# Optimization experiments

Measured on AMD Instinct MI355X. Metric: run time of the kernel, lower is better.

## Reference

```python
import jax, jax.numpy as jnp
import numpy as np

HEADS = 8
DIM_HEAD = 64
DIM = 512
NUM_BANDS = 32
MAX_FREQ = 32.0
NORM_SCALE = 10.0
RPE_DIM = (NUM_BANDS * 2 + 1) * 2  # 130


def setup_inputs() -> dict:
    key = jax.random.key(0)
    ks = jax.random.split(key, 9)
    B, N = 2, 512
    inner = HEADS * DIM_HEAD
    h2 = HEADS * 2
    inp = {
        "x": jax.random.normal(ks[0], (B, N, DIM), dtype=jnp.float32),
        "positions": jax.random.uniform(ks[1], (B, N, 2), dtype=jnp.float32),
        "W_qkv": jax.random.normal(ks[2], (DIM, 3 * inner), dtype=jnp.float32) / np.sqrt(DIM),
        "W_out": jax.random.normal(ks[3], (inner, DIM), dtype=jnp.float32) / np.sqrt(inner),
        "b_out": jnp.zeros((DIM,), dtype=jnp.float32),
        "rpe_W1": jax.random.normal(ks[4], (RPE_DIM, h2), dtype=jnp.float32) / np.sqrt(RPE_DIM),
        "rpe_b1": jnp.zeros((h2,), dtype=jnp.float32),
        "rpe_W2": jax.random.normal(ks[5], (h2, HEADS), dtype=jnp.float32) / np.sqrt(h2),
        "rpe_b2": jnp.zeros((HEADS,), dtype=jnp.float32),
    }
    return inp


def _fourier_encode(x):
    # x: [...], returns [..., 2*NUM_BANDS+1]
    freqs = jnp.linspace(1.0, MAX_FREQ, NUM_BANDS, dtype=x.dtype)
    angles = x[..., None] * freqs * jnp.pi
    return jnp.concatenate([x[..., None], jnp.sin(angles), jnp.cos(angles)], axis=-1)


def _rpe_bias(positions, W1, b1, W2, b2):
    # positions: [B, N, 2] -> bias [B, H, N, N]
    delta = positions[:, None, :, :] - positions[:, :, None, :]  # key_pos_j - query_pos_i
    dx = delta[..., 0] / NORM_SCALE
    dy = delta[..., 1] / NORM_SCALE
    dx = dx / (1.0 + jnp.abs(dx))
    dy = dy / (1.0 + jnp.abs(dy))
    feats = jnp.concatenate([_fourier_encode(dx), _fourier_encode(dy)], axis=-1)  # [B,N,N,130]
    h = jax.nn.gelu(feats @ W1 + b1, approximate=False)
    bias = h @ W2 + b2  # [B, N, N, H]
    return jnp.transpose(bias, (0, 3, 1, 2))  # [B, H, N, N]


def reference(x, positions, W_qkv, W_out, b_out, rpe_W1, rpe_b1, rpe_W2, rpe_b2):
    B, N, _ = x.shape
    H, d = HEADS, DIM_HEAD
    scale = d ** (-0.5)
    qkv = x @ W_qkv  # [B, N, 3*H*d]
    q, k, v = jnp.split(qkv, 3, axis=-1)
    q = q.reshape(B, N, H, d)
    k = k.reshape(B, N, H, d)
    v = v.reshape(B, N, H, d)
    scores = jnp.einsum('bihd,bjhd->bhij', q, k) * scale
    scores = scores + _rpe_bias(positions, rpe_W1, rpe_b1, rpe_W2, rpe_b2)
    attn = jax.nn.softmax(scores, axis=-1)
    out = jnp.einsum('bhij,bjhd->bihd', attn, v).reshape(B, N, H * d)
    return out @ W_out + b_out
```

## Files before the change

### kernel.cpp

```cpp
#include <hip/hip_runtime.h>
#include <hip/hip_fp16.h>
#include <math.h>

typedef __attribute__((ext_vector_type(8))) _Float16 f16x8;
typedef __attribute__((ext_vector_type(4))) float f32x4;

#define TBL 512
#define UMAXV (1.0f/11.0f)

__device__ __forceinline__ int swq(int row, int q) {
  return row * 64 + ((q ^ (row & 7)) << 3);
}
__device__ __forceinline__ f16x8 cvt8(float4 a, float4 b) {
  f16x8 r;
  r[0] = (_Float16)a.x; r[1] = (_Float16)a.y;
  r[2] = (_Float16)a.z; r[3] = (_Float16)a.w;
  r[4] = (_Float16)b.x; r[5] = (_Float16)b.y;
  r[6] = (_Float16)b.z; r[7] = (_Float16)b.w;
  return r;
}

__global__ __launch_bounds__(256) void k_prep(
    const float* __restrict__ Wqkv, const float* __restrict__ Wout,
    const float* __restrict__ W1, const float* __restrict__ b1,
    _Float16* __restrict__ Wt, _Float16* __restrict__ Wot,
    __half* __restrict__ Tx, __half* __restrict__ Ty) {
  __shared__ float Tt[32 * 33];
  const int t = threadIdx.x;
  const int bid = blockIdx.x;
  if (bid >= 1024) {
    int gid = (bid - 1024) * 256 + t;
    int e = gid >> 5, c = gid & 31;
    float u = -UMAXV + (2.0f * UMAXV) * (float)e / (float)(TBL - 1);
    const int xpart = (c < 16);
    const int col = c & 15;
    const int base = xpart ? 0 : 65;
    float sum = u * W1[base * 16 + col] + (xpart ? b1[col] : 0.0f);
    float s1, c1;
    sincosf(u * 3.14159265358979323846f, &s1, &c1);
    float sk = s1, ck = c1;
    for (int k = 1; k <= 32; ++k) {
      sum += sk * W1[(base + k) * 16 + col] + ck * W1[(base + 32 + k) * 16 + col];
      float ns = sk * c1 + ck * s1;
      ck = ck * c1 - sk * s1;
      sk = ns;
    }
    (xpart ? Tx : Ty)[e * 16 + col] = __float2half(sum);
    return;
  }
  int k0, n0, ncols;
  const float* W;
  _Float16* O;
  if (bid < 768) {
    k0 = (bid / 48) * 32; n0 = (bid % 48) * 32; ncols = 1536;
    W = Wqkv; O = Wt;
  } else {
    int tile = bid - 768;
    k0 = (tile / 16) * 32; n0 = (tile % 16) * 32; ncols = 512;
    W = Wout; O = Wot;
  }
  {
    int kl = t >> 3, nl = (t & 7) * 4;
    float4 v = *(const float4*)&W[(k0 + kl) * ncols + n0 + nl];
    Tt[kl * 33 + nl + 0] = v.x;
    Tt[kl * 33 + nl + 1] = v.y;
    Tt[kl * 33 + nl + 2] = v.z;
    Tt[kl * 33 + nl + 3] = v.w;
  }
  __syncthreads();
  {
    int nl = t >> 3, kq = (t & 7) * 4;
    ushort4 h;
    h.x = __builtin_bit_cast(unsigned short, (_Float16)Tt[(kq + 0) * 33 + nl]);
    h.y = __builtin_bit_cast(unsigned short, (_Float16)Tt[(kq + 1) * 33 + nl]);
    h.z = __builtin_bit_cast(unsigned short, (_Float16)Tt[(kq + 2) * 33 + nl]);
    h.w = __builtin_bit_cast(unsigned short, (_Float16)Tt[(kq + 3) * 33 + nl]);
    *(ushort4*)&O[(n0 + nl) * 512 + k0 + kq] = h;
  }
}

__global__ __launch_bounds__(512) void k_fused(
    const float* __restrict__ x, const _Float16* __restrict__ Wt,
    _Float16* __restrict__ q16, _Float16* __restrict__ k16,
    _Float16* __restrict__ vt16,
    const float* __restrict__ pos,
    const __half* __restrict__ Tx, const __half* __restrict__ Ty,
    const float* __restrict__ W2, const float* __restrict__ b2,
    _Float16* __restrict__ bias) {
  __shared__ __align__(16) unsigned short SM[16384];
  const int bid = blockIdx.x;
  const int t = threadIdx.x;

  if (bid < 192) {
    const int gb = (bid & 7) * 24 + (bid >> 3);
    _Float16* Ah = (_Float16*)SM;
    _Float16* Bh = (_Float16*)SM + 8192;
    const int mt = gb / 24, nt = gb % 24;
    const int m0 = mt * 128, n0 = nt * 64;
    const int w = t >> 6, lane = t & 63, blk = lane >> 4, jc = lane & 15;
    const int mw = (w & 3) * 32, nw = (w >> 2) * 32;
    const int sa = t >> 3, sq = t & 7;

    f32x4 acc[2][2];
    #pragma unroll
    for (int i = 0; i < 2; ++i)
      #pragma unroll
      for (int j = 0; j < 2; ++j) acc[i][j] = f32x4{0.f, 0.f, 0.f, 0.f};

    float4 pax[2][2][2];
    f16x8 pbv[2];
    #pragma unroll
    for (int s = 0; s < 2; ++s) {
      #pragma unroll
      for (int c = 0; c < 2; ++c) {
        const float* xp = &x[(m0 + sa + c * 64) * 512 + s * 64 + sq * 8];
        pax[s][c][0] = *(const float4*)xp;
        pax[s][c][1] = *(const float4*)(xp + 4);
      }
      pbv[s] = *(const f16x8*)&Wt[(n0 + sa) * 512 + s * 64 + sq * 8];
    }

    for (int it = 0; it < 8; ++it) {
      const int slot = it & 1;
      #pragma unroll
      for (int c = 0; c < 2; ++c)
        *(f16x8*)&Ah[swq(sa + c * 64, sq)] = cvt8(pax[slot][c][0], pax[slot][c][1]);
      *(f16x8*)&Bh[swq(sa, sq)] = pbv[slot];
      __syncthreads();
      if (it < 6) {
        int k0 = (it + 2) * 64;
        #pragma unroll
        for (int c = 0; c < 2; ++c) {
          const float* xp = &x[(m0 + sa + c * 64) * 512 + k0 + sq * 8];
          pax[slot][c][0] = *(const float4*)xp;
          pax[slot][c][1] = *(const float4*)(xp + 4);
        }
        pbv[slot] = *(const f16x8*)&Wt[(n0 + sa) * 512 + k0 + sq * 8];
      }
      #pragma unroll
      for (int h = 0; h < 2; ++h) {
        int q = h * 4 + blk;
        f16x8 a0 = *(const f16x8*)&Ah[swq(mw + jc, q)];
        f16x8 a1 = *(const f16x8*)&Ah[swq(mw + 16 + jc, q)];
        f16x8 b0 = *(const f16x8*)&Bh[swq(nw + jc, q)];
        f16x8 b1 = *(const f16x8*)&Bh[swq(nw + 16 + jc, q)];
        acc[0][0] = __builtin_amdgcn_mfma_f32_16x16x32_f16(a0, b0, acc[0][0], 0, 0, 0);
        acc[0][1] = __builtin_amdgcn_mfma_f32_16x16x32_f16(a0, b1, acc[0][1], 0, 0, 0);
        acc[1][0] = __builtin_amdgcn_mfma_f32_16x16x32_f16(a1, b0, acc[1][0], 0, 0, 0);
        acc[1][1] = __builtin_amdgcn_mfma_f32_16x16x32_f16(a1, b1, acc[1][1], 0, 0, 0);
      }
      __syncthreads();
    }
    const int sec = n0 >> 9;
    const int hh_ = (n0 >> 6) & 7;
    if (sec < 2) {
      _Float16* dst = (sec == 0) ? q16 : k16;
      const float scl = (sec == 0) ? 0.125f : 1.0f;
      #pragma unroll
      for (int i = 0; i < 2; ++i)
        #pragma unroll
        for (int j = 0; j < 2; ++j)
          #pragma unroll
          for (int r = 0; r < 4; ++r) {
            int tok = m0 + mw + i * 16 + blk * 4 + r;
            int b = tok >> 9, nn = tok & 511;
            int d = nw + j * 16 + jc;
            dst[((b * 8 + hh_) * 512 + nn) * 64 + d] = (_Float16)(acc[i][j][r] * scl);
          }
    } else {
      _Float16* T = (_Float16*)SM;
      #pragma unroll
      for (int i = 0; i < 2; ++i)
        #pragma unroll
        for (int j = 0; j < 2; ++j)
          #pragma unroll
          for (int r = 0; r < 4; ++r)
            T[(nw + j * 16 + jc) * 136 + mw + i * 16 + blk * 4 + r] =
                (_Float16)acc[i][j][r];
      __syncthreads();
      const int d = t >> 3, tq = t & 7;
      const int b = m0 >> 9, nb = m0 & 511;
      #pragma unroll
      for (int c = 0; c < 2; ++c) {
        int qd = tq + c * 8;
        f16x8 vv = *(const f16x8*)&T[d * 136 + qd * 8];
        *(f16x8*)&vt16[((b * 8 + hh_) * 64 + d) * 512 + nb + qd * 8] = vv;
      }
    }
    return;
  }

  const int gid = (bid - 192) * 512 + t;
  const int b = gid >> 18;
  const int i = (gid >> 9) & 511;
  const int j = gid & 511;
  const float pix = pos[(b * 512 + i) * 2 + 0];
  const float piy = pos[(b * 512 + i) * 2 + 1];
  const float pjx = pos[(b * 512 + j) * 2 + 0];
  const float pjy = pos[(b * 512 + j) * 2 + 1];
  float txv = (pjx - pix) * 0.1f; float ux = txv / (1.0f + fabsf(txv));
  float tyv = (pjy - piy) * 0.1f; float uy = tyv / (1.0f + fabsf(tyv));
  const float invstep = (float)(TBL - 1) / (2.0f * UMAXV);
  float fx = (ux + UMAXV) * invstep;
  int ix = (int)fx; ix = min(max(ix, 0), TBL - 2);
  float wx = fx - (float)ix;
  float fy = (uy + UMAXV) * invstep;
  int iy = (int)fy; iy = min(max(iy, 0), TBL - 2);
  float wy = fy - (float)iy;

  __half hx0[16], hx1[16], hy0[16], hy1[16];
  *(uint4*)&hx0[0] = *(const uint4*)&Tx[ix * 16];
  *(uint4*)&hx0[8] = *(const uint4*)&Tx[ix * 16 + 8];
  *(uint4*)&hx1[0] = *(const uint4*)&Tx[(ix + 1) * 16];
  *(uint4*)&hx1[8] = *(const uint4*)&Tx[(ix + 1) * 16 + 8];
  *(uint4*)&hy0[0] = *(const uint4*)&Ty[iy * 16];
  *(uint4*)&hy0[8] = *(const uint4*)&Ty[iy * 16 + 8];
  *(uint4*)&hy1[0] = *(const uint4*)&Ty[(iy + 1) * 16];
  *(uint4*)&hy1[8] = *(const uint4*)&Ty[(iy + 1) * 16 + 8];

  float o[8];
  #pragma unroll
  for (int c = 0; c < 8; ++c) o[c] = b2[c];
  #pragma unroll
  for (int r = 0; r < 16; ++r) {
    float ax = __half2float(hx0[r]);
    float bx = __half2float(hx1[r]);
    float ay = __half2float(hy0[r]);
    float by = __half2float(hy1[r]);
    float hv = fmaf(wx, bx - ax, ax) + fmaf(wy, by - ay, ay);
    float z = hv * 0.70710678118654752f;
    float az = fabsf(z);
    float tt = __builtin_amdgcn_rcpf(fmaf(0.3275911f, az, 1.0f));
    float poly = ((((1.061405429f * tt - 1.453152027f) * tt + 1.421413741f) * tt
                   - 0.284496736f) * tt + 0.254829592f) * tt;
    float ex = __expf(-z * z);
    float erfv = copysignf(fmaf(-poly, ex, 1.0f), z);
    float g = 0.5f * hv * (1.0f + erfv);
    #pragma unroll
    for (int c = 0; c < 8; ++c)
      o[c] = fmaf(g, W2[r * 8 + c], o[c]);
  }
  #pragma unroll
  for (int c = 0; c < 8; ++c)
    bias[((size_t)(b * 8 + c) * 512 + i) * 512 + j] = (_Float16)o[c];
}

__global__ __launch_bounds__(512) void k_attn(
    const _Float16* __restrict__ q16, const _Float16* __restrict__ k16,
    const _Float16* __restrict__ vt16, const _Float16* __restrict__ bias,
    _Float16* __restrict__ ao16) {
  __shared__ __align__(16) _Float16 psu[8 * 512];
  __shared__ __align__(16) float olds[8 * 16 * 65];
  __shared__ float mls[8 * 16 * 2];
  _Float16* bst = (_Float16*)olds;

  const int lb = (blockIdx.x & 7) * 64 + (blockIdx.x >> 3);
  const int it = lb & 31, h = (lb >> 5) & 7, b = lb >> 8;
  const int i0 = it * 16;
  const int bh = b * 8 + h;
  const int tid = threadIdx.x;
  const int w = tid >> 6, lane = tid & 63;
  const int blk = lane >> 4, jc = lane & 15;

  {
    const _Float16* bgp = bias + ((size_t)(bh * 512 + i0)) * 512;
    int brow = tid >> 5, bc = (tid & 31) * 16;
    *(f16x8*)&bst[brow * 520 + bc]     = *(const f16x8*)&bgp[brow * 512 + bc];
    *(f16x8*)&bst[brow * 520 + bc + 8] = *(const f16x8*)&bgp[brow * 512 + bc + 8];
  }

  const int qoff = (bh * 512 + i0 + jc) * 64 + blk * 8;
  const f16x8 qa0 = *(const f16x8*)&q16[qoff];
  const f16x8 qa1 = *(const f16x8*)&q16[qoff + 32];

  const int j00 = w * 64;
  f16x8 k0A0, k0A1, k0B0, k0B1, v0[4];
  {
    const int rA = (bh * 512 + j00 + jc) * 64 + blk * 8;
    const int rB = rA + 16 * 64;
    k0A0 = *(const f16x8*)&k16[rA];
    k0A1 = *(const f16x8*)&k16[rA + 32];
    k0B0 = *(const f16x8*)&k16[rB];
    k0B1 = *(const f16x8*)&k16[rB + 32];
    #pragma unroll
    for (int dt = 0; dt < 4; ++dt)
      v0[dt] = *(const f16x8*)&vt16[(bh * 64 + dt * 16 + jc) * 512 + j00 + blk * 8];
  }

  float m[4] = {-1e30f, -1e30f, -1e30f, -1e30f};
  float l[4] = {0.f, 0.f, 0.f, 0.f};
  f32x4 o[4];
  #pragma unroll
  for (int dt = 0; dt < 4; ++dt) o[dt] = f32x4{0.f, 0.f, 0.f, 0.f};

  _Float16* pw = &psu[w * 512];
  __syncthreads();

  f32x4 aA = {0.f, 0.f, 0.f, 0.f};
  aA = __builtin_amdgcn_mfma_f32_16x16x32_f16(qa0, k0A0, aA, 0, 0, 0);
  aA = __builtin_amdgcn_mfma_f32_16x16x32_f16(qa1, k0A1, aA, 0, 0, 0);
  f32x4 aB = {0.f, 0.f, 0.f, 0.f};
  aB = __builtin_amdgcn_mfma_f32_16x16x32_f16(qa0, k0B0, aB, 0, 0, 0);
  aB = __builtin_amdgcn_mfma_f32_16x16x32_f16(qa1, k0B1, aB, 0, 0, 0);

  const int j01 = w * 64 + 32;
  f16x8 k1A0, k1A1, k1B0, k1B1, v1[4];
  {
    const int rA = (bh * 512 + j01 + jc) * 64 + blk * 8;
    const int rB = rA + 16 * 64;
    k1A0 = *(const f16x8*)&k16[rA];
    k1A1 = *(const f16x8*)&k16[rA + 32];
    k1B0 = *(const f16x8*)&k16[rB];
    k1B1 = *(const f16x8*)&k16[rB + 32];
    #pragma unroll
    for (int dt = 0; dt < 4; ++dt)
      v1[dt] = *(const f16x8*)&vt16[(bh * 64 + dt * 16 + jc) * 512 + j01 + blk * 8];
  }

  {
    float sA[4], sB[4], sc[4];
    #pragma unroll
    for (int r = 0; r < 4; ++r) {
      const int br = (blk * 4 + r) * 520;
      sA[r] = aA[r] + (float)bst[br + j00 + jc];
      sB[r] = aB[r] + (float)bst[br + j00 + 16 + jc];
    }
    #pragma unroll
    for (int r = 0; r < 4; ++r) {
      float mx = fmaxf(sA[r], sB[r]);
      mx = fmaxf(mx, __shfl_xor(mx, 1, 64));
      mx = fmaxf(mx, __shfl_xor(mx, 2, 64));
      mx = fmaxf(mx, __shfl_xor(mx, 4, 64));
      mx = fmaxf(mx, __shfl_xor(mx, 8, 64));
      float mn = fmaxf(m[r], mx);
      sc[r] = __expf(m[r] - mn);
      m[r] = mn;
      float pA = __expf(sA[r] - mn);
      float pB = __expf(sB[r] - mn);
      float ps = pA + pB;
      ps += __shfl_xor(ps, 1, 64);
      ps += __shfl_xor(ps, 2, 64);
      ps += __shfl_xor(ps, 4, 64);
      ps += __shfl_xor(ps, 8, 64);
      l[r] = l[r] * sc[r] + ps;
      pw[(blk * 4 + r) * 32 + jc] = (_Float16)pA;
      pw[(blk * 4 + r) * 32 + 16 + jc] = (_Float16)pB;
    }
    #pragma unroll
    for (int dt = 0; dt < 4; ++dt)
      #pragma unroll
      for (int r = 0; r < 4; ++r)
        o[dt][r] *= sc[r];
    f16x8 pf = *(const f16x8*)&pw[jc * 32 + blk * 8];
    #pragma unroll
    for (int dt = 0; dt < 4; ++dt)
      o[dt] = __builtin_amdgcn_mfma_f32_16x16x32_f16(pf, v0[dt], o[dt], 0, 0, 0);
  }

  aA = f32x4{0.f, 0.f, 0.f, 0.f};
  aA = __builtin_amdgcn_mfma_f32_16x16x32_f16(qa0, k1A0, aA, 0, 0, 0);
  aA = __builtin_amdgcn_mfma_f32_16x16x32_f16(qa1, k1A1, aA, 0, 0, 0);
  aB = f32x4{0.f, 0.f, 0.f, 0.f};
  aB = __builtin_amdgcn_mfma_f32_16x16x32_f16(qa0, k1B0, aB, 0, 0, 0);
  aB = __builtin_amdgcn_mfma_f32_16x16x32_f16(qa1, k1B1, aB, 0, 0, 0);
  {
    float sA[4], sB[4], sc[4];
    #pragma unroll
    for (int r = 0; r < 4; ++r) {
      const int br = (blk * 4 + r) * 520;
      sA[r] = aA[r] + (float)bst[br + j01 + jc];
      sB[r] = aB[r] + (float)bst[br + j01 + 16 + jc];
    }
    #pragma unroll
    for (int r = 0; r < 4; ++r) {
      float mx = fmaxf(sA[r], sB[r]);
      mx = fmaxf(mx, __shfl_xor(mx, 1, 64));
      mx = fmaxf(mx, __shfl_xor(mx, 2, 64));
      mx = fmaxf(mx, __shfl_xor(mx, 4, 64));
      mx = fmaxf(mx, __shfl_xor(mx, 8, 64));
      float mn = fmaxf(m[r], mx);
      sc[r] = __expf(m[r] - mn);
      m[r] = mn;
      float pA = __expf(sA[r] - mn);
      float pB = __expf(sB[r] - mn);
      float ps = pA + pB;
      ps += __shfl_xor(ps, 1, 64);
      ps += __shfl_xor(ps, 2, 64);
      ps += __shfl_xor(ps, 4, 64);
      ps += __shfl_xor(ps, 8, 64);
      l[r] = l[r] * sc[r] + ps;
      pw[(blk * 4 + r) * 32 + jc] = (_Float16)pA;
      pw[(blk * 4 + r) * 32 + 16 + jc] = (_Float16)pB;
    }
    #pragma unroll
    for (int dt = 0; dt < 4; ++dt)
      #pragma unroll
      for (int r = 0; r < 4; ++r)
        o[dt][r] *= sc[r];
    f16x8 pf = *(const f16x8*)&pw[jc * 32 + blk * 8];
    #pragma unroll
    for (int dt = 0; dt < 4; ++dt)
      o[dt] = __builtin_amdgcn_mfma_f32_16x16x32_f16(pf, v1[dt], o[dt], 0, 0, 0);
  }

  __syncthreads();
  #pragma unroll
  for (int dt = 0; dt < 4; ++dt)
    #pragma unroll
    for (int r = 0; r < 4; ++r)
      olds[(w * 16 + blk * 4 + r) * 65 + dt * 16 + jc] = o[dt][r];
  if (jc == 0) {
    #pragma unroll
    for (int r = 0; r < 4; ++r) {
      mls[(w * 16 + blk * 4 + r) * 2 + 0] = m[r];
      mls[(w * 16 + blk * 4 + r) * 2 + 1] = l[r];
    }
  }
  __syncthreads();
  #pragma unroll
  for (int itx = 0; itx < 2; ++itx) {
    int idx = tid + itx * 512;
    int q = idx >> 6, d = idx & 63;
    float M = -1e30f;
    #pragma unroll
    for (int ww = 0; ww < 8; ++ww) M = fmaxf(M, mls[(ww * 16 + q) * 2]);
    float L = 0.f, acc = 0.f;
    #pragma unroll
    for (int ww = 0; ww < 8; ++ww) {
      float e = __expf(mls[(ww * 16 + q) * 2] - M);
      L += mls[(ww * 16 + q) * 2 + 1] * e;
      acc += olds[(ww * 16 + q) * 65 + d] * e;
    }
    ao16[(b * 512 + i0 + q) * 512 + h * 64 + d] = (_Float16)(acc / L);
  }
}

__global__ __launch_bounds__(256) void k_out(
    const _Float16* __restrict__ ao16, const _Float16* __restrict__ Wot,
    const float* __restrict__ bout, float* __restrict__ out) {
  __shared__ __align__(16) unsigned short SM[6144];
  _Float16* Ah = (_Float16*)SM;
  _Float16* Bh = (_Float16*)SM + 2048;

  const int lb = (blockIdx.x & 7) * 32 + (blockIdx.x >> 3);
  const int mt = lb >> 3, nt = lb & 7;
  const int m0 = mt * 32, n0 = nt * 64;
  const int t = threadIdx.x;
  const int w = t >> 6, lane = t & 63, blk = lane >> 4, jc = lane & 15;
  const int mh_ = (w & 1) * 16, nh_ = (w >> 1) * 32;
  const int sm = t >> 3, sq = t & 7;

  f32x4 acc[2];
  acc[0] = f32x4{0.f, 0.f, 0.f, 0.f};
  acc[1] = f32x4{0.f, 0.f, 0.f, 0.f};

  f16x8 pa[2], pb[2][2];
  #pragma unroll
  for (int s = 0; s < 2; ++s) {
    pa[s] = *(const f16x8*)&ao16[(m0 + sm) * 512 + s * 64 + sq * 8];
    #pragma unroll
    for (int c = 0; c < 2; ++c)
      pb[s][c] = *(const f16x8*)&Wot[(n0 + sm + c * 32) * 512 + s * 64 + sq * 8];
  }
  for (int it = 0; it < 8; ++it) {
    const int slot = it & 1;
    *(f16x8*)&Ah[swq(sm, sq)] = pa[slot];
    #pragma unroll
    for (int c = 0; c < 2; ++c)
      *(f16x8*)&Bh[swq(sm + c * 32, sq)] = pb[slot][c];
    __syncthreads();
    if (it < 6) {
      int k0 = (it + 2) * 64;
      pa[slot] = *(const f16x8*)&ao16[(m0 + sm) * 512 + k0 + sq * 8];
      #pragma unroll
      for (int c = 0; c < 2; ++c)
        pb[slot][c] = *(const f16x8*)&Wot[(n0 + sm + c * 32) * 512 + k0 + sq * 8];
    }
    #pragma unroll
    for (int h = 0; h < 2; ++h) {
      int q = h * 4 + blk;
      f16x8 a0 = *(const f16x8*)&Ah[swq(mh_ + jc, q)];
      f16x8 b0 = *(const f16x8*)&Bh[swq(nh_ + jc, q)];
      f16x8 b1 = *(const f16x8*)&Bh[swq(nh_ + 16 + jc, q)];
      acc[0] = __builtin_amdgcn_mfma_f32_16x16x32_f16(a0, b0, acc[0], 0, 0, 0);
      acc[1] = __builtin_amdgcn_mfma_f32_16x16x32_f16(a0, b1, acc[1], 0, 0, 0);
    }
    __syncthreads();
  }
  #pragma unroll
  for (int j = 0; j < 2; ++j) {
    int n = n0 + nh_ + j * 16 + jc;
    float bb = bout[n];
    #pragma unroll
    for (int r = 0; r < 4; ++r) {
      int row = m0 + mh_ + blk * 4 + r;
      out[row * 512 + n] = acc[j][r] + bb;
    }
  }
}

extern "C" void kernel_launch(void* const* d_in, const int* in_sizes, int n_in,
                              void* d_out, int out_size, void* d_ws, size_t ws_size,
                              hipStream_t stream) {
  const float* x    = (const float*)d_in[0];
  const float* pos  = (const float*)d_in[1];
  const float* Wqkv = (const float*)d_in[2];
  const float* Wout = (const float*)d_in[3];
  const float* bout = (const float*)d_in[4];
  const float* W1   = (const float*)d_in[5];
  const float* b1   = (const float*)d_in[6];
  const float* W2   = (const float*)d_in[7];
  const float* b2   = (const float*)d_in[8];
  float* out = (float*)d_out;
  char* base = (char*)d_ws;

  __half* Tx       = (__half*)(base);
  __half* Ty       = (__half*)(base + 16384);
  _Float16* Wt     = (_Float16*)(base + 32768);
  _Float16* Wot    = (_Float16*)(base + 1605632);
  _Float16* q16    = (_Float16*)(base + 2129920);
  _Float16* k16    = (_Float16*)(base + 3178496);
  _Float16* vt16   = (_Float16*)(base + 4227072);
  _Float16* bias16 = (_Float16*)(base + 5275648);
  _Float16* ao16   = (_Float16*)(base + 13664256);

  hipLaunchKernelGGL(k_prep, dim3(1088), dim3(256), 0, stream,
                     Wqkv, Wout, W1, b1, Wt, Wot, Tx, Ty);
  hipLaunchKernelGGL(k_fused, dim3(1216), dim3(512), 0, stream,
                     x, Wt, q16, k16, vt16, pos, Tx, Ty, W2, b2, bias16);
  hipLaunchKernelGGL(k_attn, dim3(512), dim3(512), 0, stream,
                     q16, k16, vt16, bias16, ao16);
  hipLaunchKernelGGL(k_out, dim3(256), dim3(256), 0, stream,
                     ao16, Wot, bout, out);
}
```

Before: 43.14 us.

## Fuse output projection into attention kernel via per-head atomic accumulation

Removes the separate output-projection kernel. Each attention block now multiplies its normalized 16x64 head output, staged in shared memory, by the matching slice of W_out and atomically adds the partial products into the fp32 output. The prep kernel gains extra blocks that pre-fill the output with the bias. This drops one launch and the ao16 round trip through global memory, but adds 8-way fp32 atomic contention per output element and a non-deterministic summation order. It also adds a launch_bounds occupancy hint of 6 to k_attn.

```diff
diff --git a/kernel.cpp b/kernel.cpp
--- a/kernel.cpp
+++ b/kernel.cpp
@@ -23,11 +23,23 @@
 __global__ __launch_bounds__(256) void k_prep(
     const float* __restrict__ Wqkv, const float* __restrict__ Wout,
     const float* __restrict__ W1, const float* __restrict__ b1,
+    const float* __restrict__ bout,
     _Float16* __restrict__ Wt, _Float16* __restrict__ Wot,
-    __half* __restrict__ Tx, __half* __restrict__ Ty) {
+    __half* __restrict__ Tx, __half* __restrict__ Ty,
+    float* __restrict__ out) {
   __shared__ float Tt[32 * 33];
   const int t = threadIdx.x;
   const int bid = blockIdx.x;
+  if (bid >= 1088) {
+    int idx16 = (bid - 1088) * 256 + t;
+    int base = idx16 * 64;
+    #pragma unroll
+    for (int c = 0; c < 16; ++c) {
+      float4 bb = *(const float4*)&bout[(base & 511) + c * 4];
+      *(float4*)&out[base + c * 4] = bb;
+    }
+    return;
+  }
   if (bid >= 1024) {
     int gid = (bid - 1024) * 256 + t;
     int e = gid >> 5, c = gid & 31;
@@ -245,10 +257,10 @@
     bias[((size_t)(b * 8 + c) * 512 + i) * 512 + j] = (_Float16)o[c];
 }
 
-__global__ __launch_bounds__(512) void k_attn(
+__global__ __launch_bounds__(512, 6) void k_attn(
     const _Float16* __restrict__ q16, const _Float16* __restrict__ k16,
     const _Float16* __restrict__ vt16, const _Float16* __restrict__ bias,
-    _Float16* __restrict__ ao16) {
+    const _Float16* __restrict__ Wot, float* __restrict__ out) {
   __shared__ __align__(16) _Float16 psu[8 * 512];
   __shared__ __align__(16) float olds[8 * 16 * 65];
   __shared__ float mls[8 * 16 * 2];
@@ -417,6 +429,7 @@
     }
   }
   __syncthreads();
+  _Float16* aof = psu;
   #pragma unroll
   for (int itx = 0; itx < 2; ++itx) {
     int idx = tid + itx * 512;
@@ -431,70 +444,30 @@
       L += mls[(ww * 16 + q) * 2 + 1] * e;
       acc += olds[(ww * 16 + q) * 65 + d] * e;
     }
-    ao16[(b * 512 + i0 + q) * 512 + h * 64 + d] = (_Float16)(acc / L);
-  }
-}
-
-__global__ __launch_bounds__(256) void k_out(
-    const _Float16* __restrict__ ao16, const _Float16* __restrict__ Wot,
-    const float* __restrict__ bout, float* __restrict__ out) {
-  __shared__ __align__(16) unsigned short SM[6144];
-  _Float16* Ah = (_Float16*)SM;
-  _Float16* Bh = (_Float16*)SM + 2048;
-
-  const int lb = (blockIdx.x & 7) * 32 + (blockIdx.x >> 3);
-  const int mt = lb >> 3, nt = lb & 7;
-  const int m0 = mt * 32, n0 = nt * 64;
-  const int t = threadIdx.x;
-  const int w = t >> 6, lane = t & 63, blk = lane >> 4, jc = lane & 15;
-  const int mh_ = (w & 1) * 16, nh_ = (w >> 1) * 32;
-  const int sm = t >> 3, sq = t & 7;
-
-  f32x4 acc[2];
-  acc[0] = f32x4{0.f, 0.f, 0.f, 0.f};
-  acc[1] = f32x4{0.f, 0.f, 0.f, 0.f};
-
-  f16x8 pa[2], pb[2][2];
-  #pragma unroll
-  for (int s = 0; s < 2; ++s) {
-    pa[s] = *(const f16x8*)&ao16[(m0 + sm) * 512 + s * 64 + sq * 8];
-    #pragma unroll
-    for (int c = 0; c < 2; ++c)
-      pb[s][c] = *(const f16x8*)&Wot[(n0 + sm + c * 32) * 512 + s * 64 + sq * 8];
-  }
-  for (int it = 0; it < 8; ++it) {
-    const int slot = it & 1;
-    *(f16x8*)&Ah[swq(sm, sq)] = pa[slot];
-    #pragma unroll
-    for (int c = 0; c < 2; ++c)
-      *(f16x8*)&Bh[swq(sm + c * 32, sq)] = pb[slot][c];
-    __syncthreads();
-    if (it < 6) {
-      int k0 = (it + 2) * 64;
-      pa[slot] = *(const f16x8*)&ao16[(m0 + sm) * 512 + k0 + sq * 8];
-      #pragma unroll
-      for (int c = 0; c < 2; ++c)
-        pb[slot][c] = *(const f16x8*)&Wot[(n0 + sm + c * 32) * 512 + k0 + sq * 8];
-    }
-    #pragma unroll
-    for (int h = 0; h < 2; ++h) {
-      int q = h * 4 + blk;
-      f16x8 a0 = *(const f16x8*)&Ah[swq(mh_ + jc, q)];
-      f16x8 b0 = *(const f16x8*)&Bh[swq(nh_ + jc, q)];
-      f16x8 b1 = *(const f16x8*)&Bh[swq(nh_ + 16 + jc, q)];
-      acc[0] = __builtin_amdgcn_mfma_f32_16x16x32_f16(a0, b0, acc[0], 0, 0, 0);
-      acc[1] = __builtin_amdgcn_mfma_f32_16x16x32_f16(a0, b1, acc[1], 0, 0, 0);
-    }
-    __syncthreads();
-  }
-  #pragma unroll
-  for (int j = 0; j < 2; ++j) {
-    int n = n0 + nh_ + j * 16 + jc;
-    float bb = bout[n];
+    aof[q * 64 + (((d >> 3) ^ (q & 7)) << 3) + (d & 7)] = (_Float16)(acc / L);
+  }
+  __syncthreads();
+
+  f32x4 acc2[4];
+  #pragma unroll
+  for (int ns = 0; ns < 4; ++ns) acc2[ns] = f32x4{0.f, 0.f, 0.f, 0.f};
+  #pragma unroll
+  for (int ks = 0; ks < 2; ++ks) {
+    const f16x8 af = *(const f16x8*)&aof[swq(jc, ks * 4 + blk)];
+    #pragma unroll
+    for (int ns = 0; ns < 4; ++ns) {
+      const f16x8 bf =
+          *(const f16x8*)&Wot[(w * 64 + ns * 16 + jc) * 512 + h * 64 + ks * 32 + blk * 8];
+      acc2[ns] = __builtin_amdgcn_mfma_f32_16x16x32_f16(af, bf, acc2[ns], 0, 0, 0);
+    }
+  }
+  #pragma unroll
+  for (int ns = 0; ns < 4; ++ns) {
+    const int n = w * 64 + ns * 16 + jc;
     #pragma unroll
     for (int r = 0; r < 4; ++r) {
-      int row = m0 + mh_ + blk * 4 + r;
-      out[row * 512 + n] = acc[j][r] + bb;
+      const int row = i0 + blk * 4 + r;
+      atomicAdd(&out[(b * 512 + row) * 512 + n], acc2[ns][r]);
     }
   }
 }
@@ -522,14 +495,11 @@
   _Float16* k16    = (_Float16*)(base + 3178496);
   _Float16* vt16   = (_Float16*)(base + 4227072);
   _Float16* bias16 = (_Float16*)(base + 5275648);
-  _Float16* ao16   = (_Float16*)(base + 13664256);
-
-  hipLaunchKernelGGL(k_prep, dim3(1088), dim3(256), 0, stream,
-                     Wqkv, Wout, W1, b1, Wt, Wot, Tx, Ty);
+
+  hipLaunchKernelGGL(k_prep, dim3(1120), dim3(256), 0, stream,
+                     Wqkv, Wout, W1, b1, bout, Wt, Wot, Tx, Ty, out);
   hipLaunchKernelGGL(k_fused, dim3(1216), dim3(512), 0, stream,
                      x, Wt, q16, k16, vt16, pos, Tx, Ty, W2, b2, bias16);
   hipLaunchKernelGGL(k_attn, dim3(512), dim3(512), 0, stream,
-                     q16, k16, vt16, bias16, ao16);
-  hipLaunchKernelGGL(k_out, dim3(256), dim3(256), 0, stream,
-                     ao16, Wot, bout, out);
+                     q16, k16, vt16, bias16, Wot, out);
 }
```

Measured after the change: 55.72 us. +29.2%, slower.
